# Performance work log

Hardware: AMD Instinct MI355X
Metric: run time of the kernel (lower is better)

The kernel has to match this reference:

```python
import jax, jax.numpy as jnp
import numpy as np


def _cif_cmat(w_seq):
    """Integrate-and-fire assignment matrix for one sequence.
    w_seq: [T] sigmoid weights. Returns [T, T+1] (T+1 is a static upper
    bound on the number of fired output frames)."""
    T = w_seq.shape[0]
    cols = jnp.arange(T + 1)

    def step(carry, w):
        acc, k = carry
        fire = acc + w > 1.0
        on_k = (cols == k).astype(w.dtype)
        on_k1 = (cols == k + 1).astype(w.dtype)
        row_fire = on_k * (1.0 - acc) / w + on_k1 * (acc + w - 1.0) / w
        row = jnp.where(fire, row_fire, on_k)
        acc_new = jnp.where(fire, jnp.zeros_like(acc), acc + w)  # original resets acc to 0
        k_new = jnp.where(fire, k + 1, k)
        return (acc_new, k_new), row

    init = (jnp.zeros((), w_seq.dtype), jnp.zeros((), jnp.int32))
    _, rows = jax.lax.scan(step, init, w_seq)
    return rows  # [T, T+1]


def setup_inputs() -> dict:
    key = jax.random.key(0)
    k1, k2, k3 = jax.random.split(key, 3)
    B, T, D = 8, 2000, 512
    feat = jax.random.normal(k1, (B, T, D), dtype=jnp.float32)
    hlens = jax.random.randint(k2, (B,), 0, T).astype(jnp.int32)
    W = jax.random.normal(k3, (D,), dtype=jnp.float32) * (1.0 / np.sqrt(D))
    b = jnp.zeros((1,), dtype=jnp.float32)
    return {"feat": feat, "hlens": hlens, "W": W, "b": b}


def reference(feat, hlens, W, b):
    # weight = sigmoid(Linear(feat))  -> [B, T]
    weight = jax.nn.sigmoid(jnp.einsum("btd,d->bt", feat, W) + b[0])
    hlens_new = jnp.ceil(jnp.sum(weight, axis=1)).astype(jnp.int32)
    # sequential integrate-and-fire scan, vmapped over batch -> [B, T, T+1]
    weight_cmat = jax.lax.stop_gradient(jax.vmap(_cif_cmat)(weight))
    weight_mat = weight[:, :, None] * weight_cmat        # [B, T, M]
    feat_new = jnp.einsum("btd,btm->bmd", feat, weight_mat)  # [B, M, D]
    return feat_new, hlens_new
```

## Files before the change

### kernel.cpp

```cpp
#include <hip/hip_runtime.h>
#include <math.h>

#define BATCH 8
#define TLEN 2000
#define DIM 512
#define MLEN (TLEN + 1)
#define NTH 1024
#define MAXLVL 11

__global__ __launch_bounds__(256) void weight_kernel(
    const float* __restrict__ feat, const float* __restrict__ W,
    const float* __restrict__ bias, float* __restrict__ weight) {
  int gwave = (blockIdx.x * 256 + threadIdx.x) >> 6;
  int lane  = threadIdx.x & 63;
  if (gwave >= BATCH * TLEN) return;
  const float4* f4 = (const float4*)feat + (size_t)gwave * (DIM / 4) + lane * 2;
  const float4* w4 = (const float4*)W + lane * 2;
  float4 a0 = f4[0], a1 = f4[1];
  float4 b0 = w4[0], b1 = w4[1];
  float s = a0.x * b0.x + a0.y * b0.y + a0.z * b0.z + a0.w * b0.w +
            a1.x * b1.x + a1.y * b1.y + a1.z * b1.z + a1.w * b1.w;
#pragma unroll
  for (int off = 32; off > 0; off >>= 1) s += __shfl_xor(s, off, 64);
  if (lane == 0) {
    float x = s + bias[0];
    weight[gwave] = 1.0f / (1.0f + expf(-x));
  }
}

__global__ __launch_bounds__(NTH) void scan_kernel(
    const float* __restrict__ weight, float* __restrict__ hlens_out,
    int4* __restrict__ AB) {
  int b = blockIdx.x;
  int tid = threadIdx.x;
  int lane = tid & 63, wid = tid >> 6;

  __shared__ float w_s[TLEN];
  __shared__ float S_s[TLEN];
  __shared__ float wtot[16];
  __shared__ unsigned short Ga_s[MLEN];
  __shared__ unsigned short Gb_s[MLEN];
  __shared__ unsigned short F_s[2048];
  __shared__ int done_lv[MAXLVL];
  __shared__ int K_s;

  const float* wrow = weight + b * TLEN;
  int base = tid * 2;
  float w0 = 0.f, w1 = 0.f;
  if (base < TLEN) {
    float2 v = *(const float2*)(wrow + base);
    w0 = v.x; w1 = v.y;
  }
  float mysum = w0 + w1;
  float sc = mysum;
#pragma unroll
  for (int d = 1; d < 64; d <<= 1) {
    float o = __shfl_up(sc, d, 64);
    if (lane >= d) sc += o;
  }
  if (lane == 63) wtot[wid] = sc;
  if (tid < MAXLVL) done_lv[tid] = 1;
  __syncthreads();
  float woff = 0.f;
  for (int j = 0; j < wid; j++) woff += wtot[j];
  float excl = woff + (sc - mysum);
  if (base < TLEN) {
    w_s[base] = w0; w_s[base + 1] = w1;
    S_s[base] = excl + w0;
    S_s[base + 1] = excl + w0 + w1;
  }
  if (tid == 0) {
    float tot = 0.f;
    for (int j = 0; j < 16; j++) tot += wtot[j];
    hlens_out[b] = ceilf(tot);
  }
  __syncthreads();

  {
    int l0 = tid + 1, r0 = TLEN;  float tg0 = S_s[tid] + 1.0f;
    int s1v = tid + 1024;
    bool has1 = (s1v < TLEN);
    int l1 = has1 ? s1v + 1 : TLEN, r1 = TLEN;
    float tg1 = has1 ? S_s[s1v] + 1.0f : 0.f;
    bool has2 = (tid == 0);
    int l2 = 0, r2 = has2 ? TLEN : 0;
#pragma unroll
    for (int step = 0; step < MAXLVL; step++) {
      if (l0 < r0) { int m = (l0 + r0) >> 1; if (S_s[m] > tg0) r0 = m; else l0 = m + 1; }
      if (l1 < r1) { int m = (l1 + r1) >> 1; if (S_s[m] > tg1) r1 = m; else l1 = m + 1; }
      if (l2 < r2) { int m = (l2 + r2) >> 1; if (S_s[m] > 1.0f) r2 = m; else l2 = m + 1; }
    }
    Ga_s[tid] = (unsigned short)l0;
    if (has1) Ga_s[s1v] = (unsigned short)l1;
    F_s[tid] = (unsigned short)TLEN;
    F_s[tid + 1024] = (unsigned short)TLEN;
    if (tid == 0) {
      Ga_s[TLEN] = (unsigned short)TLEN;
      F_s[0] = (unsigned short)l2;
    }
  }
  __syncthreads();

  {
    unsigned short* cur = Ga_s;
    unsigned short* nxt = Gb_s;
    int flen = 1;
    for (int lvl = 0; lvl < MAXLVL; lvl++) {
      int s0 = tid, s1v = tid + 1024;
      int g20 = (int)cur[cur[s0]];
      int g21 = (s1v <= TLEN) ? (int)cur[cur[s1v]] : TLEN;
      int i0 = tid, i1 = tid + 1024;
      int nv0 = -1, nv1 = -1;
      if (i0 < flen) nv0 = (int)cur[F_s[i0]];
      if (i1 < flen) nv1 = (int)cur[F_s[i1]];
      nxt[s0] = (unsigned short)g20;
      if (s1v <= TLEN) nxt[s1v] = (unsigned short)g21;
      if (i0 < flen) { F_s[flen + i0] = (unsigned short)nv0; if (nv0 < TLEN) done_lv[lvl] = 0; }
      if (i1 < flen) { F_s[flen + i1] = (unsigned short)nv1; if (nv1 < TLEN) done_lv[lvl] = 0; }
      __syncthreads();
      flen <<= 1;
      unsigned short* t = cur; cur = nxt; nxt = t;
      if (done_lv[lvl]) break;
    }
  }

#pragma unroll
  for (int it = 0; it < 2; it++) {
    int k = tid + it * 1024;
    if ((int)F_s[k] == TLEN && (k == 0 || (int)F_s[k - 1] < TLEN)) K_s = k;
  }
  __syncthreads();
  int K = K_s;

#pragma unroll
  for (int it = 0; it < 2; it++) {
    int m = tid + it * 1024;
    if (m >= MLEN) continue;
    int a, e;
    float cL = 0.f, cR = 0.f;
    if (m == 0) {
      a = 0;
      if (K > 0) {
        e = (int)F_s[0];
        cR = 1.0f - ((e > 0) ? S_s[e - 1] : 0.f);
      } else {
        e = TLEN - 1;
        cR = w_s[TLEN - 1];
      }
    } else if (m <= K) {
      int f1 = (int)F_s[m - 1];
      float Sp0 = (m >= 2) ? S_s[(int)F_s[m - 2]] : 0.f;
      a = f1;
      cL = S_s[f1] - Sp0 - 1.0f;
      if (m < K) {
        e = (int)F_s[m];
        cR = 1.0f - (S_s[e - 1] - S_s[f1]);
      } else {
        e = TLEN - 1;
        cR = w_s[TLEN - 1];
      }
    } else {
      a = 0x7fffffff; e = -1;
    }
    int4 pk;
    pk.x = a; pk.y = e;
    pk.z = __float_as_int(cL);
    pk.w = __float_as_int(cR);
    AB[(size_t)b * MLEN + m] = pk;
  }
}

__global__ __launch_bounds__(256) void gather_kernel(
    const float* __restrict__ feat, const float* __restrict__ weight,
    const int4* __restrict__ AB, float* __restrict__ out) {
  int bm = (blockIdx.x * 256 + threadIdx.x) >> 6;
  int lane = threadIdx.x & 63;
  if (bm >= BATCH * MLEN) return;
  int b = bm / MLEN, m = bm % MLEN;
  int4 ab = AB[(size_t)bm];
  int a = ab.x, e = ab.y;
  float cL = __int_as_float(ab.z), cR = __int_as_float(ab.w);
  float4 acc0 = {0.f, 0.f, 0.f, 0.f};
  float4 acc1 = {0.f, 0.f, 0.f, 0.f};
  const float4* f4 = (const float4*)feat + (size_t)b * TLEN * (DIM / 4) + lane * 2;
  const float* wrow = weight + b * TLEN;
  for (int t = a; t <= e; t++) {
    float c = (t == a && m > 0) ? cL : ((t == e) ? cR : wrow[t]);
    const float4* fr = f4 + (size_t)t * (DIM / 4);
    float4 fa = fr[0], fb = fr[1];
    acc0.x += c * fa.x; acc0.y += c * fa.y; acc0.z += c * fa.z; acc0.w += c * fa.w;
    acc1.x += c * fb.x; acc1.y += c * fb.y; acc1.z += c * fb.z; acc1.w += c * fb.w;
  }
  float4* orow = (float4*)out + (size_t)bm * (DIM / 4) + lane * 2;
  orow[0] = acc0;
  orow[1] = acc1;
}

extern "C" void kernel_launch(void* const* d_in, const int* in_sizes, int n_in,
                              void* d_out, int out_size, void* d_ws, size_t ws_size,
                              hipStream_t stream) {
  const float* feat = (const float*)d_in[0];
  const float* W    = (const float*)d_in[2];
  const float* bias = (const float*)d_in[3];

  float* out       = (float*)d_out;
  float* feat_new  = out;
  float* hlens_out = out + (size_t)BATCH * MLEN * DIM;

  char* ws = (char*)d_ws;
  float* weight = (float*)ws;
  int4*  AB     = (int4*)(ws + 64000);

  weight_kernel<<<(BATCH * TLEN) / 4, 256, 0, stream>>>(feat, W, bias, weight);
  scan_kernel<<<BATCH, NTH, 0, stream>>>(weight, hlens_out, AB);
  int nframes = BATCH * MLEN;
  gather_kernel<<<(nframes + 3) / 4, 256, 0, stream>>>(feat, weight, AB, feat_new);
}
```

Before: 100.1 us.

## Use radix-4 pointer jumping with fixed levels in CIF scan kernel

Replaces the radix-2 pointer-jumping loop in the scan kernel with a radix-4 scheme. Each level follows three successor hops and runs a fixed five levels, with no per-level done flag and no separate K search. It relies on a bound that fires are at least two steps apart, since weights are below 1. That bound caps fired frames at 1000 and lets the binary search start at t+2. The aim is fewer barrier rounds and less shared-memory bookkeeping in the serial per-batch kernel, at the cost of always running all levels instead of exiting early.

```diff
diff --git a/kernel.cpp b/kernel.cpp
--- a/kernel.cpp
+++ b/kernel.cpp
@@ -6,7 +6,7 @@
 #define DIM 512
 #define MLEN (TLEN + 1)
 #define NTH 1024
-#define MAXLVL 11
+#define KMAX 1000
 
 __global__ __launch_bounds__(256) void weight_kernel(
     const float* __restrict__ feat, const float* __restrict__ W,
@@ -40,9 +40,7 @@
   __shared__ float wtot[16];
   __shared__ unsigned short Ga_s[MLEN];
   __shared__ unsigned short Gb_s[MLEN];
-  __shared__ unsigned short F_s[2048];
-  __shared__ int done_lv[MAXLVL];
-  __shared__ int K_s;
+  __shared__ unsigned short F_s[1024];
 
   const float* wrow = weight + b * TLEN;
   int base = tid * 2;
@@ -59,7 +57,6 @@
     if (lane >= d) sc += o;
   }
   if (lane == 63) wtot[wid] = sc;
-  if (tid < MAXLVL) done_lv[tid] = 1;
   __syncthreads();
   float woff = 0.f;
   for (int j = 0; j < wid; j++) woff += wtot[j];
@@ -77,23 +74,22 @@
   __syncthreads();
 
   {
-    int l0 = tid + 1, r0 = TLEN;  float tg0 = S_s[tid] + 1.0f;
+    int l0 = (tid + 2 < TLEN) ? tid + 2 : TLEN, r0 = TLEN;
+    float tg0 = S_s[tid] + 1.0f;
     int s1v = tid + 1024;
     bool has1 = (s1v < TLEN);
-    int l1 = has1 ? s1v + 1 : TLEN, r1 = TLEN;
+    int l1 = has1 ? ((s1v + 2 < TLEN) ? s1v + 2 : TLEN) : TLEN, r1 = TLEN;
     float tg1 = has1 ? S_s[s1v] + 1.0f : 0.f;
     bool has2 = (tid == 0);
     int l2 = 0, r2 = has2 ? TLEN : 0;
 #pragma unroll
-    for (int step = 0; step < MAXLVL; step++) {
+    for (int step = 0; step < 11; step++) {
       if (l0 < r0) { int m = (l0 + r0) >> 1; if (S_s[m] > tg0) r0 = m; else l0 = m + 1; }
       if (l1 < r1) { int m = (l1 + r1) >> 1; if (S_s[m] > tg1) r1 = m; else l1 = m + 1; }
       if (l2 < r2) { int m = (l2 + r2) >> 1; if (S_s[m] > 1.0f) r2 = m; else l2 = m + 1; }
     }
     Ga_s[tid] = (unsigned short)l0;
     if (has1) Ga_s[s1v] = (unsigned short)l1;
-    F_s[tid] = (unsigned short)TLEN;
-    F_s[tid + 1024] = (unsigned short)TLEN;
     if (tid == 0) {
       Ga_s[TLEN] = (unsigned short)TLEN;
       F_s[0] = (unsigned short)l2;
@@ -105,32 +101,32 @@
     unsigned short* cur = Ga_s;
     unsigned short* nxt = Gb_s;
     int flen = 1;
-    for (int lvl = 0; lvl < MAXLVL; lvl++) {
-      int s0 = tid, s1v = tid + 1024;
-      int g20 = (int)cur[cur[s0]];
-      int g21 = (s1v <= TLEN) ? (int)cur[cur[s1v]] : TLEN;
-      int i0 = tid, i1 = tid + 1024;
-      int nv0 = -1, nv1 = -1;
-      if (i0 < flen) nv0 = (int)cur[F_s[i0]];
-      if (i1 < flen) nv1 = (int)cur[F_s[i1]];
-      nxt[s0] = (unsigned short)g20;
-      if (s1v <= TLEN) nxt[s1v] = (unsigned short)g21;
-      if (i0 < flen) { F_s[flen + i0] = (unsigned short)nv0; if (nv0 < TLEN) done_lv[lvl] = 0; }
-      if (i1 < flen) { F_s[flen + i1] = (unsigned short)nv1; if (nv1 < TLEN) done_lv[lvl] = 0; }
+#pragma unroll
+    for (int lvl = 0; lvl < 5; lvl++) {
+      if (tid < flen) {
+        int e1 = (int)cur[(int)F_s[tid]];
+        int e2 = (int)cur[e1];
+        int e3 = (int)cur[e2];
+        F_s[flen + tid] = (unsigned short)e1;
+        F_s[2 * flen + tid] = (unsigned short)e2;
+        F_s[3 * flen + tid] = (unsigned short)e3;
+      }
+      if (lvl < 4) {
+        int a0 = (int)cur[tid];
+        a0 = (int)cur[a0]; a0 = (int)cur[a0]; a0 = (int)cur[a0];
+        nxt[tid] = (unsigned short)a0;
+        int s1v = tid + 1024;
+        if (s1v <= TLEN) {
+          int a1 = (int)cur[s1v];
+          a1 = (int)cur[a1]; a1 = (int)cur[a1]; a1 = (int)cur[a1];
+          nxt[s1v] = (unsigned short)a1;
+        }
+      }
       __syncthreads();
-      flen <<= 1;
+      flen <<= 2;
       unsigned short* t = cur; cur = nxt; nxt = t;
-      if (done_lv[lvl]) break;
-    }
-  }
-
-#pragma unroll
-  for (int it = 0; it < 2; it++) {
-    int k = tid + it * 1024;
-    if ((int)F_s[k] == TLEN && (k == 0 || (int)F_s[k - 1] < TLEN)) K_s = k;
-  }
-  __syncthreads();
-  int K = K_s;
+    }
+  }
 
 #pragma unroll
   for (int it = 0; it < 2; it++) {
@@ -140,20 +136,22 @@
     float cL = 0.f, cR = 0.f;
     if (m == 0) {
       a = 0;
-      if (K > 0) {
-        e = (int)F_s[0];
+      int f0 = (int)F_s[0];
+      if (f0 < TLEN) {
+        e = f0;
         cR = 1.0f - ((e > 0) ? S_s[e - 1] : 0.f);
       } else {
         e = TLEN - 1;
         cR = w_s[TLEN - 1];
       }
-    } else if (m <= K) {
+    } else if (m <= KMAX && (int)F_s[m - 1] < TLEN) {
       int f1 = (int)F_s[m - 1];
       float Sp0 = (m >= 2) ? S_s[(int)F_s[m - 2]] : 0.f;
       a = f1;
       cL = S_s[f1] - Sp0 - 1.0f;
-      if (m < K) {
-        e = (int)F_s[m];
+      int fm = (int)F_s[m];
+      if (fm < TLEN) {
+        e = fm;
         cR = 1.0f - (S_s[e - 1] - S_s[f1]);
       } else {
         e = TLEN - 1;
```

Result: no change. 99.82 us (-0.3%).
